# Kernel optimization log

Measured on AMD Instinct MI355X. Metric: run time of the kernel, lower is better.

## Reference

```python
import jax, jax.numpy as jnp
import numpy as np

B, N, C = 8, 2048, 512

def setup_inputs() -> dict:
    key = jax.random.key(0)
    k1, k2, k3 = jax.random.split(key, 3)
    x = jax.random.normal(k1, (B, N, C), dtype=jnp.float32)
    # xavier_uniform with gain=1.414 ~ uniform(-b, b), b = gain*sqrt(6/(fan_in+fan_out))
    bw = 1.414 * np.sqrt(6.0 / (C + C))
    w = jax.random.uniform(k2, (C, C), dtype=jnp.float32, minval=-bw, maxval=bw)
    ba = 1.414 * np.sqrt(6.0 / (2 * C + 1))
    a = jax.random.uniform(k3, (2 * C, 1), dtype=jnp.float32, minval=-ba, maxval=ba)
    return {"x": x, "w": w, "a": a}

def reference(x, w, a):
    # x: [B,N,C], w: [C,C], a: [2C,1]
    C_ = w.shape[0]
    h = jnp.matmul(x, w)                      # [B,N,C]
    a1 = a[:C_, 0]                            # [C]
    a2 = a[C_:, 0]                            # [C]
    # The torch repeat/cat/view builds e_ij = LeakyReLU(a1.h_i + a2.h_j);
    # compute the same math via broadcasting (no [B,N,N,2C] tensor).
    s1 = jnp.einsum('bnc,c->bn', h, a1)       # [B,N]
    s2 = jnp.einsum('bnc,c->bn', h, a2)       # [B,N]
    e = jax.nn.leaky_relu(s1[:, :, None] + s2[:, None, :], negative_slope=0.2)  # [B,N,N]
    attention = jax.nn.softmax(e, axis=2)     # softmax over source nodes j
    # dropout is identity in eval mode (training=False)
    h_prime = jnp.matmul(attention, x)        # [B,N,C]
    return h_prime
```

## Files before the change

kernel.cpp:

```cpp
#include <hip/hip_runtime.h>
#include <math.h>

#define B_ 8
#define N_ 2048
#define C_ 512
#define G_ 32
#define L_ 64

static const size_t OFF_V1   = 0;
static const size_t OFF_V2   = OFF_V1 + 512;
static const size_t OFF_S1   = OFF_V2 + 512;
static const size_t OFF_S2   = OFF_S1 + 16384;
static const size_t OFF_Z    = OFF_S2 + 16384;
static const size_t OFF_IDX  = OFF_Z + 16384;
static const size_t OFF_P    = OFF_IDX + 16384;
static const size_t OFF_Q    = OFF_P + 16384;
static const size_t OFF_CHP  = OFF_Q + 16384;
static const size_t OFF_CHQ  = OFF_CHP + 131072;
static const size_t OFF_TOTQ = OFF_CHQ + 131072;
static const size_t OFF_FP   = OFF_TOTQ + 4096;
static const size_t OFF_FQ   = OFF_FP + 16384;
static const size_t OFF_ROWS = OFF_FQ + 16384;
static const size_t OFF_POS  = OFF_ROWS + 16384;

__global__ __launch_bounds__(64) void k_wa(const float* __restrict__ w,
                                           const float* __restrict__ a,
                                           float* __restrict__ v1, float* __restrict__ v2) {
    int k = blockIdx.x, lane = threadIdx.x;
    float acc1 = 0.f, acc2 = 0.f;
    for (int c = lane; c < C_; c += 64) {
        float wv = w[k * C_ + c];
        acc1 += wv * a[c];
        acc2 += wv * a[C_ + c];
    }
    for (int o = 32; o > 0; o >>= 1) { acc1 += __shfl_down(acc1, o); acc2 += __shfl_down(acc2, o); }
    if (lane == 0) { v1[k] = acc1; v2[k] = acc2; }
}

__global__ __launch_bounds__(256) void k_s(const float* __restrict__ x,
                                           const float* __restrict__ v1,
                                           const float* __restrict__ v2,
                                           float* __restrict__ s1, float* __restrict__ s2) {
    __shared__ __align__(16) float sv1[C_];
    __shared__ __align__(16) float sv2[C_];
    int tid = threadIdx.x;
    for (int c = tid; c < C_; c += 256) { sv1[c] = v1[c]; sv2[c] = v2[c]; }
    __syncthreads();
    int wave = tid >> 6, lane = tid & 63;
    int r = blockIdx.x * 4 + wave;
    const float4* xr  = reinterpret_cast<const float4*>(x + (size_t)r * C_);
    const float4* w1p = reinterpret_cast<const float4*>(sv1);
    const float4* w2p = reinterpret_cast<const float4*>(sv2);
    float a1 = 0.f, a2 = 0.f;
    for (int half = 0; half < 2; ++half) {
        int c4 = lane + half * 64;
        float4 xv = xr[c4], w1 = w1p[c4], w2 = w2p[c4];
        a1 += xv.x*w1.x + xv.y*w1.y + xv.z*w1.z + xv.w*w1.w;
        a2 += xv.x*w2.x + xv.y*w2.y + xv.z*w2.z + xv.w*w2.w;
    }
    for (int o = 32; o > 0; o >>= 1) { a1 += __shfl_down(a1, o); a2 += __shfl_down(a2, o); }
    if (lane == 0) { s1[r] = a1; s2[r] = a2; }
}

__global__ __launch_bounds__(256) void k_rank(const float* __restrict__ s2,
                                              float* __restrict__ z, int* __restrict__ idxArr,
                                              float* __restrict__ pArr, float* __restrict__ qArr) {
    __shared__ float sval[N_];
    __shared__ float sred[256];
    __shared__ int   srnk[256];
    int blk = blockIdx.x;
    int b = blk >> 5, grp = blk & 31;
    int tid = threadIdx.x;
    int le = tid & 63, qtr = tid >> 6;
    for (int i = tid; i < N_; i += 256) sval[i] = s2[(size_t)b * N_ + i];
    __syncthreads();
    int e = grp * 64 + le;
    float val = sval[e];
    int base = qtr * 512;
    int rank = 0;
    float mx = -3.4e38f;
    #pragma unroll 8
    for (int i = 0; i < 512; ++i) {
        int t = base + i;
        float v = sval[t];
        mx = fmaxf(mx, v);
        rank += (v < val) || (v == val && t < e);
    }
    srnk[tid] = rank;
    sred[tid] = mx;
    __syncthreads();
    for (int o = 128; o > 0; o >>= 1) {
        if (tid < o) sred[tid] = fmaxf(sred[tid], sred[tid + o]);
        __syncthreads();
    }
    float m2 = sred[0];
    if (qtr == 0) {
        int rk = srnk[le] + srnk[le + 64] + srnk[le + 128] + srnk[le + 192];
        float d = val - m2;
        size_t pos = (size_t)b * N_ + rk;
        z[pos]      = val;
        idxArr[pos] = e;
        pArr[pos]   = __expf(d);
        qArr[pos]   = __expf(0.2f * d);
    }
}

__global__ __launch_bounds__(512) void k_chunk(const float* __restrict__ x,
                                               const int* __restrict__ idxArr,
                                               const float* __restrict__ pArr,
                                               const float* __restrict__ qArr,
                                               float* __restrict__ chP, float* __restrict__ chQ) {
    int bg = blockIdx.x, b = bg >> 5, g = bg & 31;
    int c = threadIdx.x;
    __shared__ int   srow[L_];
    __shared__ float spv[L_], sqv[L_];
    if (c < L_) {
        int j = g * L_ + c;
        srow[c] = idxArr[b * N_ + j];
        spv[c]  = pArr[b * N_ + j];
        sqv[c]  = qArr[b * N_ + j];
    }
    __syncthreads();
    const float* xb = x + (size_t)b * N_ * C_;
    float accP = 0.f, accQ = 0.f;
    for (int t = 0; t < L_; ++t) {
        float xv = xb[(size_t)srow[t] * C_ + c];
        accP += spv[t] * xv;
        accQ += sqv[t] * xv;
    }
    chP[(size_t)bg * C_ + c] = accP;
    chQ[(size_t)bg * C_ + c] = accQ;
}

__global__ __launch_bounds__(1024) void k_prep(const float* __restrict__ s1,
                                               const float* __restrict__ z,
                                               const float* __restrict__ pArr,
                                               const float* __restrict__ qArr,
                                               float* __restrict__ chP,
                                               float* __restrict__ chQ,
                                               float* __restrict__ totQ,
                                               float* __restrict__ fPArr,
                                               float* __restrict__ fQArr,
                                               int* __restrict__ rowsSorted,
                                               int* __restrict__ posStart) {
    __shared__ float Ppre[2049], Qpre[2049];
    __shared__ float zv[N_];
    __shared__ int   cnt[2049];
    __shared__ int   ps[2050];
    __shared__ float wsP[16], wsQ[16], woP[16], woQ[16];
    __shared__ int   wsC[16], woC[16];
    int b = blockIdx.x, tid = threadIdx.x, lane = tid & 63, wid = tid >> 6;
    size_t ib = (size_t)b * N_;

    for (int i = tid; i < 2049; i += 1024) cnt[i] = 0;
    zv[2*tid]   = z[ib + 2*tid];
    zv[2*tid+1] = z[ib + 2*tid+1];

    float p0 = pArr[ib + 2*tid], p1 = pArr[ib + 2*tid+1];
    float q0 = qArr[ib + 2*tid], q1 = qArr[ib + 2*tid+1];
    float pv = p0 + p1, qv = q0 + q1;
    float pi = pv, qi = qv;
    for (int o = 1; o < 64; o <<= 1) {
        float tp = __shfl_up(pi, o), tq2 = __shfl_up(qi, o);
        if (lane >= o) { pi += tp; qi += tq2; }
    }
    if (lane == 63) { wsP[wid] = pi; wsQ[wid] = qi; }
    __syncthreads();
    if (wid == 0 && lane < 16) {
        float sp = wsP[lane], sq = wsQ[lane];
        float ip = sp, iq = sq;
        for (int o = 1; o < 16; o <<= 1) {
            float tp = __shfl_up(ip, o), tq2 = __shfl_up(iq, o);
            if (lane >= o) { ip += tp; iq += tq2; }
        }
        woP[lane] = ip - sp; woQ[lane] = iq - sq;
    }
    {
        int c = tid & 511, sel = tid >> 9;
        float* arr = sel ? chQ : chP;
        float v[G_];
        #pragma unroll
        for (int g = 0; g < G_; ++g)
            v[g] = arr[((size_t)(b * G_ + g)) * C_ + c];
        float run = 0.f;
        #pragma unroll
        for (int g = G_ - 1; g >= 0; --g) {
            float t = v[g];
            arr[((size_t)(b * G_ + g)) * C_ + c] = run;
            run += t;
        }
        if (sel) totQ[b * C_ + c] = run;
    }
    __syncthreads();
    float inclP = pi + woP[wid], inclQ = qi + woQ[wid];
    float exclP = inclP - pv,    exclQ = inclQ - qv;
    Ppre[2*tid]   = exclP;  Ppre[2*tid+1] = exclP + p0;
    Qpre[2*tid]   = exclQ;  Qpre[2*tid+1] = exclQ + q0;
    if (tid == 1023) { Ppre[2048] = inclP; Qpre[2048] = inclQ; }
    __syncthreads();

    float m2   = zv[N_ - 1];
    float Ptot = Ppre[2048];
    int kk[2], sl[2];
    #pragma unroll
    for (int h = 0; h < 2; ++h) {
        int rl = tid + h * 1024;
        float s1v = s1[ib + rl];
        float thr = -s1v;
        int lo = 0, hi = N_;
        while (lo < hi) { int mid = (lo + hi) >> 1; if (zv[mid] >= thr) hi = mid; else lo = mid + 1; }
        float beta = s1v + m2;
        float wPc, wQc;
        if (beta >= 0.f) { wPc = 1.f;                  wQc = __expf(-0.8f * beta); }
        else             { wPc = __expf(0.8f * beta);  wQc = 1.f; }
        float Sp = Ptot - Ppre[lo];
        float Sq = Qpre[lo];
        float inv = 1.f / (wPc * Sp + wQc * Sq);
        fPArr[ib + rl] = wPc * inv;
        fQArr[ib + rl] = wQc * inv;
        kk[h] = lo;
        sl[h] = atomicAdd(&cnt[lo], 1);
    }
    __syncthreads();

    int c0 = cnt[2*tid], c1 = cnt[2*tid+1];
    int cv = c0 + c1, ci = cv;
    for (int o = 1; o < 64; o <<= 1) {
        int t = __shfl_up(ci, o);
        if (lane >= o) ci += t;
    }
    if (lane == 63) wsC[wid] = ci;
    __syncthreads();
    if (wid == 0 && lane < 16) {
        int sc = wsC[lane], ic = sc;
        for (int o = 1; o < 16; o <<= 1) { int t = __shfl_up(ic, o); if (lane >= o) ic += t; }
        woC[lane] = ic - sc;
    }
    __syncthreads();
    int inclC = ci + woC[wid];
    int exclC = inclC - cv;
    ps[2*tid] = exclC; ps[2*tid+1] = exclC + c0;
    if (tid == 1023) { ps[2048] = inclC; ps[2049] = inclC + cnt[2048]; }
    __syncthreads();
    posStart[b * 2050 + tid]        = ps[tid];
    posStart[b * 2050 + 1024 + tid] = ps[1024 + tid];
    if (tid < 2) posStart[b * 2050 + 2048 + tid] = ps[2048 + tid];
    #pragma unroll
    for (int h = 0; h < 2; ++h) {
        int rl = tid + h * 1024;
        rowsSorted[ib + ps[kk[h]] + sl[h]] = rl;
    }
}

__global__ __launch_bounds__(512) void k_fused(const float* __restrict__ x,
                                               const int* __restrict__ idxArr,
                                               const float* __restrict__ pArr,
                                               const float* __restrict__ qArr,
                                               const float* __restrict__ chP,
                                               const float* __restrict__ chQ,
                                               const float* __restrict__ totQ,
                                               const float* __restrict__ fPArr,
                                               const float* __restrict__ fQArr,
                                               const int* __restrict__ rowsSorted,
                                               const int* __restrict__ posStart,
                                               float* __restrict__ out) {
    int bg = blockIdx.x, b = bg >> 5, g = bg & 31;
    int c = threadIdx.x;
    __shared__ int   srow[L_];
    __shared__ float spv[L_], sqv[L_];
    __shared__ int   sps[66];
    if (c < L_) {
        int j = g * L_ + c;
        srow[c] = idxArr[b * N_ + j];
        spv[c]  = pArr[b * N_ + j];
        sqv[c]  = qArr[b * N_ + j];
    }
    if (c < 66) sps[c] = posStart[b * 2050 + g * L_ + c];
    __syncthreads();
    const float* xb  = x + (size_t)b * N_ * C_;
    const float* fPb = fPArr + (size_t)b * N_;
    const float* fQb = fQArr + (size_t)b * N_;
    const int*   rs  = rowsSorted + (size_t)b * N_;
    float*       ob  = out + (size_t)b * N_ * C_;
    float runP = chP[(size_t)bg * C_ + c];
    float runQ = chQ[(size_t)bg * C_ + c];
    float tq   = totQ[b * C_ + c];
    if (g == G_ - 1) {
        for (int u = sps[64]; u < sps[65]; ++u) {
            int r = rs[u];
            ob[(size_t)r * C_ + c] = fPb[r] * runP + fQb[r] * (tq - runQ);
        }
    }
    float xv_next = xb[(size_t)srow[L_ - 1] * C_ + c];
    for (int t = L_ - 1; t >= 0; --t) {
        float xv = xv_next;
        if (t > 0) xv_next = xb[(size_t)srow[t - 1] * C_ + c];
        runP = fmaf(spv[t], xv, runP);
        runQ = fmaf(sqv[t], xv, runQ);
        for (int u = sps[t]; u < sps[t + 1]; ++u) {
            int r = rs[u];
            ob[(size_t)r * C_ + c] = fPb[r] * runP + fQb[r] * (tq - runQ);
        }
    }
}

extern "C" void kernel_launch(void* const* d_in, const int* in_sizes, int n_in,
                              void* d_out, int out_size, void* d_ws, size_t ws_size,
                              hipStream_t stream) {
    const float* x = (const float*)d_in[0];
    const float* w = (const float*)d_in[1];
    const float* a = (const float*)d_in[2];
    float* out = (float*)d_out;
    float* ws  = (float*)d_ws;

    float* v1   = ws + OFF_V1;
    float* v2   = ws + OFF_V2;
    float* s1   = ws + OFF_S1;
    float* s2   = ws + OFF_S2;
    float* zArr = ws + OFF_Z;
    int*   idxA = (int*)(ws + OFF_IDX);
    float* pArr = ws + OFF_P;
    float* qArr = ws + OFF_Q;
    float* chP  = ws + OFF_CHP;
    float* chQ  = ws + OFF_CHQ;
    float* totQ = ws + OFF_TOTQ;
    float* fPA  = ws + OFF_FP;
    float* fQA  = ws + OFF_FQ;
    int*   rows = (int*)(ws + OFF_ROWS);
    int*   pos  = (int*)(ws + OFF_POS);

    k_wa   <<<dim3(C_),      dim3(64),   0, stream>>>(w, a, v1, v2);
    k_s    <<<dim3(4096),    dim3(256),  0, stream>>>(x, v1, v2, s1, s2);
    k_rank <<<dim3(B_ * 32), dim3(256),  0, stream>>>(s2, zArr, idxA, pArr, qArr);
    k_chunk<<<dim3(B_ * G_), dim3(512),  0, stream>>>(x, idxA, pArr, qArr, chP, chQ);
    k_prep <<<dim3(B_),      dim3(1024), 0, stream>>>(s1, zArr, pArr, qArr, chP, chQ, totQ,
                                                      fPA, fQA, rows, pos);
    k_fused<<<dim3(B_ * G_), dim3(512),  0, stream>>>(x, idxA, pArr, qArr, chP, chQ, totQ,
                                                      fPA, fQA, rows, pos, out);
}
```

Before: 152.3 us.

## Halve chunk length, batch gathered row loads, stage emit metadata in LDS

Chunk count doubles (G 32→64, L 64→32), so k_chunk and k_fused launch twice as many blocks with half the serial scan length each. Both kernels now gather all L rows of x into registers up front, replacing the serial one-at-a-time loads. k_prep writes each output row's fP/fQ coefficients in emission order alongside the row index, and k_fused stages a chunk's emit list into shared memory before scanning. This targets latency-bound serial gathers and scattered global reads, at the cost of more register pressure and a 24KB shared staging buffer that may reduce occupancy.

```diff
diff --git a/kernel.cpp b/kernel.cpp
--- a/kernel.cpp
+++ b/kernel.cpp
@@ -4,8 +4,8 @@
 #define B_ 8
 #define N_ 2048
 #define C_ 512
-#define G_ 32
-#define L_ 64
+#define G_ 64
+#define L_ 32
 
 static const size_t OFF_V1   = 0;
 static const size_t OFF_V2   = OFF_V1 + 512;
@@ -16,12 +16,12 @@
 static const size_t OFF_P    = OFF_IDX + 16384;
 static const size_t OFF_Q    = OFF_P + 16384;
 static const size_t OFF_CHP  = OFF_Q + 16384;
-static const size_t OFF_CHQ  = OFF_CHP + 131072;
-static const size_t OFF_TOTQ = OFF_CHQ + 131072;
-static const size_t OFF_FP   = OFF_TOTQ + 4096;
-static const size_t OFF_FQ   = OFF_FP + 16384;
-static const size_t OFF_ROWS = OFF_FQ + 16384;
-static const size_t OFF_POS  = OFF_ROWS + 16384;
+static const size_t OFF_CHQ  = OFF_CHP + 262144;
+static const size_t OFF_TOTQ = OFF_CHQ + 262144;
+static const size_t OFF_EMR  = OFF_TOTQ + 4096;
+static const size_t OFF_EMP  = OFF_EMR + 16384;
+static const size_t OFF_EMQ  = OFF_EMP + 16384;
+static const size_t OFF_POS  = OFF_EMQ + 16384;
 
 __global__ __launch_bounds__(64) void k_wa(const float* __restrict__ w,
                                            const float* __restrict__ a,
@@ -52,6 +52,7 @@
     const float4* w1p = reinterpret_cast<const float4*>(sv1);
     const float4* w2p = reinterpret_cast<const float4*>(sv2);
     float a1 = 0.f, a2 = 0.f;
+    #pragma unroll
     for (int half = 0; half < 2; ++half) {
         int c4 = lane + half * 64;
         float4 xv = xr[c4], w1 = w1p[c4], w2 = w2p[c4];
@@ -110,7 +111,7 @@
                                                const float* __restrict__ pArr,
                                                const float* __restrict__ qArr,
                                                float* __restrict__ chP, float* __restrict__ chQ) {
-    int bg = blockIdx.x, b = bg >> 5, g = bg & 31;
+    int bg = blockIdx.x, b = bg >> 6, g = bg & 63;
     int c = threadIdx.x;
     __shared__ int   srow[L_];
     __shared__ float spv[L_], sqv[L_];
@@ -122,11 +123,14 @@
     }
     __syncthreads();
     const float* xb = x + (size_t)b * N_ * C_;
+    float xr_[L_];
+    #pragma unroll
+    for (int t = 0; t < L_; ++t) xr_[t] = xb[(size_t)srow[t] * C_ + c];
     float accP = 0.f, accQ = 0.f;
+    #pragma unroll
     for (int t = 0; t < L_; ++t) {
-        float xv = xb[(size_t)srow[t] * C_ + c];
-        accP += spv[t] * xv;
-        accQ += sqv[t] * xv;
+        accP = fmaf(spv[t], xr_[t], accP);
+        accQ = fmaf(sqv[t], xr_[t], accQ);
     }
     chP[(size_t)bg * C_ + c] = accP;
     chQ[(size_t)bg * C_ + c] = accQ;
@@ -139,9 +143,9 @@
                                                float* __restrict__ chP,
                                                float* __restrict__ chQ,
                                                float* __restrict__ totQ,
-                                               float* __restrict__ fPArr,
-                                               float* __restrict__ fQArr,
-                                               int* __restrict__ rowsSorted,
+                                               int* __restrict__ emRow,
+                                               float* __restrict__ emFP,
+                                               float* __restrict__ emFQ,
                                                int* __restrict__ posStart) {
     __shared__ float Ppre[2049], Qpre[2049];
     __shared__ float zv[N_];
@@ -201,7 +205,8 @@
 
     float m2   = zv[N_ - 1];
     float Ptot = Ppre[2048];
-    int kk[2], sl[2];
+    int   kk[2], sl[2];
+    float fPv[2], fQv[2];
     #pragma unroll
     for (int h = 0; h < 2; ++h) {
         int rl = tid + h * 1024;
@@ -216,8 +221,8 @@
         float Sp = Ptot - Ppre[lo];
         float Sq = Qpre[lo];
         float inv = 1.f / (wPc * Sp + wQc * Sq);
-        fPArr[ib + rl] = wPc * inv;
-        fQArr[ib + rl] = wQc * inv;
+        fPv[h] = wPc * inv;
+        fQv[h] = wQc * inv;
         kk[h] = lo;
         sl[h] = atomicAdd(&cnt[lo], 1);
     }
@@ -248,7 +253,10 @@
     #pragma unroll
     for (int h = 0; h < 2; ++h) {
         int rl = tid + h * 1024;
-        rowsSorted[ib + ps[kk[h]] + sl[h]] = rl;
+        int u  = ps[kk[h]] + sl[h];
+        emRow[ib + u] = rl;
+        emFP [ib + u] = fPv[h];
+        emFQ [ib + u] = fQv[h];
     }
 }
 
@@ -259,47 +267,57 @@
                                                const float* __restrict__ chP,
                                                const float* __restrict__ chQ,
                                                const float* __restrict__ totQ,
-                                               const float* __restrict__ fPArr,
-                                               const float* __restrict__ fQArr,
-                                               const int* __restrict__ rowsSorted,
+                                               const int* __restrict__ emRow,
+                                               const float* __restrict__ emFP,
+                                               const float* __restrict__ emFQ,
                                                const int* __restrict__ posStart,
                                                float* __restrict__ out) {
-    int bg = blockIdx.x, b = bg >> 5, g = bg & 31;
+    int bg = blockIdx.x, b = bg >> 6, g = bg & 63;
     int c = threadIdx.x;
     __shared__ int   srow[L_];
     __shared__ float spv[L_], sqv[L_];
-    __shared__ int   sps[66];
+    __shared__ int   sps[L_ + 2];
+    __shared__ int   semRow[N_];
+    __shared__ float semFP[N_], semFQ[N_];
     if (c < L_) {
         int j = g * L_ + c;
         srow[c] = idxArr[b * N_ + j];
         spv[c]  = pArr[b * N_ + j];
         sqv[c]  = qArr[b * N_ + j];
     }
-    if (c < 66) sps[c] = posStart[b * 2050 + g * L_ + c];
-    __syncthreads();
-    const float* xb  = x + (size_t)b * N_ * C_;
-    const float* fPb = fPArr + (size_t)b * N_;
-    const float* fQb = fQArr + (size_t)b * N_;
-    const int*   rs  = rowsSorted + (size_t)b * N_;
-    float*       ob  = out + (size_t)b * N_ * C_;
+    if (c < L_ + 2) sps[c] = posStart[b * 2050 + g * L_ + c];
+    __syncthreads();
+    int uStart = sps[0];
+    int uEnd   = (g == G_ - 1) ? sps[L_ + 1] : sps[L_];
+    size_t ib = (size_t)b * N_;
+    for (int u = uStart + c; u < uEnd; u += 512) {
+        int e = u - uStart;
+        semRow[e] = emRow[ib + u];
+        semFP[e]  = emFP [ib + u];
+        semFQ[e]  = emFQ [ib + u];
+    }
+    __syncthreads();
+    const float* xb = x + (size_t)b * N_ * C_;
+    float*       ob = out + (size_t)b * N_ * C_;
+    float xr_[L_];
+    #pragma unroll
+    for (int t = 0; t < L_; ++t) xr_[t] = xb[(size_t)srow[t] * C_ + c];
     float runP = chP[(size_t)bg * C_ + c];
     float runQ = chQ[(size_t)bg * C_ + c];
     float tq   = totQ[b * C_ + c];
     if (g == G_ - 1) {
-        for (int u = sps[64]; u < sps[65]; ++u) {
-            int r = rs[u];
-            ob[(size_t)r * C_ + c] = fPb[r] * runP + fQb[r] * (tq - runQ);
+        for (int u = sps[L_]; u < sps[L_ + 1]; ++u) {
+            int e = u - uStart;
+            ob[(size_t)semRow[e] * C_ + c] = semFP[e] * runP + semFQ[e] * (tq - runQ);
         }
     }
-    float xv_next = xb[(size_t)srow[L_ - 1] * C_ + c];
+    #pragma unroll
     for (int t = L_ - 1; t >= 0; --t) {
-        float xv = xv_next;
-        if (t > 0) xv_next = xb[(size_t)srow[t - 1] * C_ + c];
-        runP = fmaf(spv[t], xv, runP);
-        runQ = fmaf(sqv[t], xv, runQ);
+        runP = fmaf(spv[t], xr_[t], runP);
+        runQ = fmaf(sqv[t], xr_[t], runQ);
         for (int u = sps[t]; u < sps[t + 1]; ++u) {
-            int r = rs[u];
-            ob[(size_t)r * C_ + c] = fPb[r] * runP + fQb[r] * (tq - runQ);
+            int e = u - uStart;
+            ob[(size_t)semRow[e] * C_ + c] = semFP[e] * runP + semFQ[e] * (tq - runQ);
         }
     }
 }
@@ -324,9 +342,9 @@
     float* chP  = ws + OFF_CHP;
     float* chQ  = ws + OFF_CHQ;
     float* totQ = ws + OFF_TOTQ;
-    float* fPA  = ws + OFF_FP;
-    float* fQA  = ws + OFF_FQ;
-    int*   rows = (int*)(ws + OFF_ROWS);
+    int*   emR  = (int*)(ws + OFF_EMR);
+    float* emP  = ws + OFF_EMP;
+    float* emQ  = ws + OFF_EMQ;
     int*   pos  = (int*)(ws + OFF_POS);
 
     k_wa   <<<dim3(C_),      dim3(64),   0, stream>>>(w, a, v1, v2);
@@ -334,7 +352,7 @@
     k_rank <<<dim3(B_ * 32), dim3(256),  0, stream>>>(s2, zArr, idxA, pArr, qArr);
     k_chunk<<<dim3(B_ * G_), dim3(512),  0, stream>>>(x, idxA, pArr, qArr, chP, chQ);
     k_prep <<<dim3(B_),      dim3(1024), 0, stream>>>(s1, zArr, pArr, qArr, chP, chQ, totQ,
-                                                      fPA, fQA, rows, pos);
+                                                      emR, emP, emQ, pos);
     k_fused<<<dim3(B_ * G_), dim3(512),  0, stream>>>(x, idxA, pArr, qArr, chP, chQ, totQ,
-                                                      fPA, fQA, rows, pos, out);
-}
+                                                      emR, emP, emQ, pos, out);
+}
```

Measured after the change: 140.3 us. 1.09x faster.
